# Optimization experiments

Measured on AMD Instinct MI355X. Metric: run time of the kernel, lower is better.

## Reference

```python
import jax, jax.numpy as jnp
import numpy as np

B, S, NX, NH = 4, 1024, 1024, 16
HD = NX // NH  # 64


def setup_inputs() -> dict:
    key = jax.random.key(0)
    k1, k2, k3 = jax.random.split(key, 3)
    return {
        "hidden_states": jax.random.normal(k1, (B, S, NX), dtype=jnp.float32),
        "c_attn_w": jax.random.normal(k2, (NX, 3 * NX), dtype=jnp.float32) * 0.02,
        "c_attn_b": jnp.zeros((3 * NX,), dtype=jnp.float32),
        "c_proj_w": jax.random.normal(k3, (NX, NX), dtype=jnp.float32) * 0.02,
        "c_proj_b": jnp.zeros((NX,), dtype=jnp.float32),
    }


def reference(hidden_states, c_attn_w, c_attn_b, c_proj_w, c_proj_b):
    # Conv1D fused QKV projection: x @ W + b, then split into q,k,v
    qkv = hidden_states @ c_attn_w + c_attn_b  # [B,S,3*NX]
    q, k, v = jnp.split(qkv, 3, axis=-1)
    # split heads -> [B, H, S, D]
    def heads(x):
        return x.reshape(B, S, NH, HD).transpose(0, 2, 1, 3)
    q, k, v = heads(q), heads(k), heads(v)
    # scores: q @ k^T / sqrt(D)  (scale=True; NOTE: no causal mask in this fork)
    w = jnp.einsum("bhqd,bhkd->bhqk", q, k) / jnp.sqrt(jnp.asarray(HD, q.dtype))
    w = jax.nn.softmax(w, axis=-1)
    a = jnp.einsum("bhqk,bhkd->bhqd", w, v)  # [B,H,S,D]
    # merge heads -> [B,S,NX]
    a = a.transpose(0, 2, 1, 3).reshape(B, S, NX)
    # output projection (dropout is identity in eval)
    return a @ c_proj_w + c_proj_b
```

## Files before the change

kernel.cpp:

```cpp
#include <hip/hip_runtime.h>
#include <hip/hip_fp16.h>
#include <cmath>

constexpr int Bb  = 4;
constexpr int Ss  = 1024;
constexpr int NXc = 1024;
constexpr int NHc = 16;
constexpr int HDc = 64;

typedef __bf16    bf16x8 __attribute__((ext_vector_type(8)));
typedef _Float16  f16x8  __attribute__((ext_vector_type(8)));
typedef float     f32x4  __attribute__((ext_vector_type(4)));
typedef unsigned short ushortT;
typedef ushortT ushort8v __attribute__((ext_vector_type(8)));

#define QSCALE 0.18033688011112042f

__device__ __forceinline__ ushortT f2bf_rne(float x) {
  unsigned u = __float_as_uint(x);
  unsigned r = (u + 0x7FFFu + ((u >> 16) & 1u)) >> 16;
  return (ushortT)r;
}
__device__ __forceinline__ ushortT f2h_bits(float x) {
  return __half_as_ushort(__float2half(x));
}
__device__ __forceinline__ float h2f(ushortT h) {
  return __half2float(__ushort_as_half(h));
}
__device__ __forceinline__ void split_f16(float x, ushortT& hi, ushortT& lo) {
  hi = f2h_bits(x);
  lo = f2h_bits(x - h2f(hi));
}

__device__ __forceinline__ void gll16(const void* g, void* l) {
  __builtin_amdgcn_global_load_lds(
      (const __attribute__((address_space(1))) unsigned int*)g,
      (__attribute__((address_space(3))) unsigned int*)l, 16, 0, 0);
}

__device__ __forceinline__ void drain_vmem() {
  asm volatile("s_waitcnt vmcnt(0)" ::: "memory");
  __builtin_amdgcn_sched_barrier(0);
}

__global__ __launch_bounds__(256) void prep_all(
    const float* __restrict__ hs, const float* __restrict__ aw,
    const float* __restrict__ pw,
    ushortT* __restrict__ hF, ushortT* __restrict__ awT,
    ushortT* __restrict__ pwT)
{
  const int bid = blockIdx.x;
  if (bid < 4096) {
    int i = (bid * 256 + threadIdx.x) * 4;
    float4 v = *reinterpret_cast<const float4*>(&hs[i]);
    *reinterpret_cast<ushort4*>(&hF[i]) =
        make_ushort4(f2h_bits(v.x), f2h_bits(v.y), f2h_bits(v.z), f2h_bits(v.w));
    return;
  }
  __shared__ float tile[32][33];
  const int tx = threadIdx.x & 31, ty = threadIdx.x >> 5;
  if (bid < 7168) {
    const int b2 = bid - 4096;
    const int n0 = (b2 % 96) * 32, k0 = (b2 / 96) * 32;
    #pragma unroll
    for (int i = 0; i < 4; ++i)
      tile[ty + i * 8][tx] = aw[(size_t)(k0 + ty + i * 8) * 3072 + n0 + tx];
    __syncthreads();
    #pragma unroll
    for (int i = 0; i < 4; ++i)
      awT[(size_t)(n0 + ty + i * 8) * 1024 + k0 + tx] = f2h_bits(tile[tx][ty + i * 8]);
  } else {
    const int b2 = bid - 7168;
    const int n0 = (b2 & 31) * 32, k0 = (b2 >> 5) * 32;
    #pragma unroll
    for (int i = 0; i < 4; ++i)
      tile[ty + i * 8][tx] = pw[(size_t)(k0 + ty + i * 8) * 1024 + n0 + tx];
    __syncthreads();
    #pragma unroll
    for (int i = 0; i < 4; ++i)
      pwT[(size_t)(n0 + ty + i * 8) * 1024 + k0 + tx] = f2h_bits(tile[tx][ty + i * 8]);
  }
}

__global__ __launch_bounds__(256) void gemm_f16_qkv(
    const ushortT* __restrict__ A16, const ushortT* __restrict__ B16,
    const float* __restrict__ bias,
    ushortT* __restrict__ Qb, ushortT* __restrict__ Kb,
    ushortT* __restrict__ Vt, int M, int N, int K)
{
  constexpr int BK = 64;
  __shared__ ushortT smem[32768];

  const int t    = threadIdx.x;
  const int lane = t & 63;
  const int w    = t >> 6;
  const int wr   = w >> 1, wc = w & 1;
  const int m0 = blockIdx.y * 128;
  const int n0 = blockIdx.x * 128;
  const int l15 = lane & 15;
  const int g   = lane >> 4;

  const int srow  = w * 32 + (lane >> 3);
  const int sslot = (lane & 7) ^ (lane >> 3);

  f32x4 acc[4][4];
  #pragma unroll
  for (int m = 0; m < 4; ++m)
    #pragma unroll
    for (int n = 0; n < 4; ++n)
      #pragma unroll
      for (int r = 0; r < 4; ++r) acc[m][n][r] = 0.f;

  const ushortT* pA = A16 + (size_t)(m0 + srow) * K + sslot * 8;
  const ushortT* pB = B16 + (size_t)(n0 + srow) * K + sslot * 8;

  auto STAGE = [&](ushortT* buf, int k0) {
    #pragma unroll
    for (int i = 0; i < 4; ++i) {
      const size_t gstep = (size_t)i * 8 * K + k0;
      const int    loff  = (w * 32 + i * 8) * BK;
      gll16(pA + gstep, &buf[loff]);
      gll16(pB + gstep, &buf[8192 + loff]);
    }
  };

  const int arow = wr * 64 + l15;
  const int bcol = wc * 64 + l15;

  auto COMPUTE = [&](const ushortT* buf) {
    const ushortT* sA = buf;
    const ushortT* sB = buf + 8192;
    #pragma unroll
    for (int c = 0; c < 2; ++c) {
      const int slot = c * 4 + g;
      f16x8 af[4], bf[4];
      #pragma unroll
      for (int m = 0; m < 4; ++m) {
        int r   = arow + m * 16;
        int off = r * BK + ((slot ^ (r & 7)) * 8);
        af[m] = *reinterpret_cast<const f16x8*>(&sA[off]);
      }
      #pragma unroll
      for (int n = 0; n < 4; ++n) {
        int r   = bcol + n * 16;
        int off = r * BK + ((slot ^ (r & 7)) * 8);
        bf[n] = *reinterpret_cast<const f16x8*>(&sB[off]);
      }
      #pragma unroll
      for (int m = 0; m < 4; ++m)
        #pragma unroll
        for (int n = 0; n < 4; ++n)
          acc[m][n] = __builtin_amdgcn_mfma_f32_16x16x32_f16(af[m], bf[n], acc[m][n], 0, 0, 0);
    }
  };

  const int nt = K / BK;
  STAGE(&smem[0], 0);
  drain_vmem();
  __syncthreads();
  for (int tt = 0; tt < nt; tt += 2) {
    if (tt + 1 < nt) STAGE(&smem[16384], (tt + 1) * BK);
    COMPUTE(&smem[0]);
    drain_vmem();
    __syncthreads();
    if (tt + 2 < nt) STAGE(&smem[0], (tt + 2) * BK);
    COMPUTE(&smem[16384]);
    drain_vmem();
    __syncthreads();
  }

  const int region = n0 >> 10;
  if (region < 2) {
    #pragma unroll
    for (int n = 0; n < 4; ++n) {
      int col_g = n0 + wc * 64 + n * 16 + l15;
      int colm  = col_g & 1023;
      float bv  = bias[col_g];
      #pragma unroll
      for (int m = 0; m < 4; ++m) {
        int row = m0 + wr * 64 + m * 16 + (g << 2);
        #pragma unroll
        for (int r = 0; r < 4; ++r) {
          float v = acc[m][n][r] + bv;
          if (region == 0)
            Qb[(size_t)(row + r) * 1024 + colm] = f2bf_rne(v * QSCALE);
          else
            Kb[(size_t)(row + r) * 1024 + colm] = f2bf_rne(v);
        }
      }
    }
  } else {
    ushortT* T = smem;
    #pragma unroll
    for (int n = 0; n < 4; ++n) {
      int cl   = wc * 64 + n * 16 + l15;
      float bv = bias[n0 + cl];
      #pragma unroll
      for (int m = 0; m < 4; ++m) {
        int rl = wr * 64 + m * 16 + (g << 2);
        #pragma unroll
        for (int r = 0; r < 4; ++r)
          T[cl * 136 + rl + r] = f2bf_rne(acc[m][n][r] + bv);
      }
    }
    __syncthreads();
    const int c  = t >> 1;
    const int rh = (t & 1) * 64;
    const int nn = (n0 - 2048) + c;
    const int hh = nn >> 6, dd = nn & 63;
    const int bb = m0 >> 10;
    const int sl = (m0 & 1023) + rh;
    size_t vbase = ((size_t)((bb * 16 + hh) * 64 + dd)) * 1024 + sl;
    #pragma unroll
    for (int j = 0; j < 8; ++j) {
      ushort8v v = *reinterpret_cast<const ushort8v*>(&T[c * 136 + rh + j * 8]);
      *reinterpret_cast<ushort8v*>(&Vt[vbase + j * 8]) = v;
    }
  }
}

__global__ __launch_bounds__(256) void gemm_f16p2(
    const ushortT* __restrict__ Ah, const ushortT* __restrict__ Al,
    const ushortT* __restrict__ B16,
    const float* __restrict__ bias, float* __restrict__ C,
    int M, int N, int K)
{
  constexpr int BK = 64;
  __shared__ ushortT smem[3 * 8192];
  ushortT* sAh = smem;
  ushortT* sAl = smem + 8192;
  ushortT* sB  = smem + 16384;

  const int t    = threadIdx.x;
  const int lane = t & 63;
  const int w    = t >> 6;
  const int wr   = w >> 1, wc = w & 1;
  const int m0 = blockIdx.y * 128;
  const int n0 = blockIdx.x * 128;
  const int l15 = lane & 15;
  const int g   = lane >> 4;

  const int srow  = w * 32 + (lane >> 3);
  const int sslot = (lane & 7) ^ (lane >> 3);

  f32x4 acc[4][4];
  #pragma unroll
  for (int m = 0; m < 4; ++m)
    #pragma unroll
    for (int n = 0; n < 4; ++n)
      #pragma unroll
      for (int r = 0; r < 4; ++r) acc[m][n][r] = 0.f;

  const ushortT* pAh = Ah  + (size_t)(m0 + srow) * K + sslot * 8;
  const ushortT* pAl = Al  + (size_t)(m0 + srow) * K + sslot * 8;
  const ushortT* pB  = B16 + (size_t)(n0 + srow) * K + sslot * 8;

  for (int k0 = 0; k0 < K; k0 += BK) {
    #pragma unroll
    for (int i = 0; i < 4; ++i) {
      const size_t gstep = (size_t)i * 8 * K + k0;
      const int    loff  = (w * 32 + i * 8) * BK;
      gll16(pAh + gstep, &sAh[loff]);
      gll16(pAl + gstep, &sAl[loff]);
      gll16(pB  + gstep, &sB[loff]);
    }
    __syncthreads();

    const int arow = wr * 64 + l15;
    const int bcol = wc * 64 + l15;
    #pragma unroll
    for (int c = 0; c < 2; ++c) {
      const int slot = c * 4 + g;
      f16x8 afh[4], afl[4], bf[4];
      #pragma unroll
      for (int m = 0; m < 4; ++m) {
        int r   = arow + m * 16;
        int off = r * BK + ((slot ^ (r & 7)) * 8);
        afh[m] = *reinterpret_cast<const f16x8*>(&sAh[off]);
        afl[m] = *reinterpret_cast<const f16x8*>(&sAl[off]);
      }
      #pragma unroll
      for (int n = 0; n < 4; ++n) {
        int r   = bcol + n * 16;
        int off = r * BK + ((slot ^ (r & 7)) * 8);
        bf[n] = *reinterpret_cast<const f16x8*>(&sB[off]);
      }
      #pragma unroll
      for (int m = 0; m < 4; ++m)
        #pragma unroll
        for (int n = 0; n < 4; ++n) {
          acc[m][n] = __builtin_amdgcn_mfma_f32_16x16x32_f16(afh[m], bf[n], acc[m][n], 0, 0, 0);
          acc[m][n] = __builtin_amdgcn_mfma_f32_16x16x32_f16(afl[m], bf[n], acc[m][n], 0, 0, 0);
        }
    }
    __syncthreads();
  }

  #pragma unroll
  for (int n = 0; n < 4; ++n) {
    int col  = n0 + wc * 64 + n * 16 + l15;
    float bv = bias[col];
    #pragma unroll
    for (int m = 0; m < 4; ++m) {
      int row = m0 + wr * 64 + m * 16 + (g << 2);
      #pragma unroll
      for (int r = 0; r < 4; ++r)
        C[(size_t)(row + r) * N + col] = acc[m][n][r] + bv;
    }
  }
}

__global__ __launch_bounds__(256) void attn_mfma(
    const ushortT* __restrict__ Qb, const ushortT* __restrict__ Kb,
    const ushortT* __restrict__ Vt,
    ushortT* __restrict__ aHi, ushortT* __restrict__ aLo)
{
  __shared__ ushortT sK[64 * 64];
  __shared__ ushortT sV[64 * 64];
  __shared__ ushortT sP[64 * 64];

  const int t    = threadIdx.x;
  const int lane = t & 63;
  const int w    = t >> 6;
  const int bh = blockIdx.x, b = bh >> 4, h = bh & 15;
  const int q0 = blockIdx.y * 64;
  const int l15 = lane & 15;
  const int g   = lane >> 4;

  bf16x8 qa[2];
  #pragma unroll
  for (int ks = 0; ks < 2; ++ks) {
    size_t addr = (size_t)(b * 1024 + q0 + w * 16 + l15) * 1024
                  + h * 64 + ks * 32 + g * 8;
    qa[ks] = *reinterpret_cast<const bf16x8*>(&Qb[addr]);
  }

  const int srow  = lane >> 3;
  const int sslot = (lane & 7) ^ srow;

  f32x4 O[4];
  float lp[4];
  #pragma unroll
  for (int r = 0; r < 4; ++r) lp[r] = 0.f;
  #pragma unroll
  for (int n = 0; n < 4; ++n)
    #pragma unroll
    for (int r = 0; r < 4; ++r) O[n][r] = 0.f;

  for (int kt = 0; kt < 16; ++kt) {
    const int k0 = kt * 64;
    #pragma unroll
    for (int i = 0; i < 2; ++i) {
      int r = w * 16 + i * 8 + srow;
      gll16(&Kb[(size_t)(b * 1024 + k0 + r) * 1024 + h * 64 + sslot * 8],
            &sK[(w * 16 + i * 8) * 64]);
      gll16(&Vt[((size_t)bh * 64 + r) * 1024 + k0 + sslot * 8],
            &sV[(w * 16 + i * 8) * 64]);
    }
    __syncthreads();

    f32x4 sc[4];
    #pragma unroll
    for (int n = 0; n < 4; ++n)
      #pragma unroll
      for (int r = 0; r < 4; ++r) sc[n][r] = 0.f;

    #pragma unroll
    for (int ks = 0; ks < 2; ++ks) {
      bf16x8 kb[4];
      #pragma unroll
      for (int n = 0; n < 4; ++n) {
        int row = n * 16 + l15;
        kb[n] = *reinterpret_cast<const bf16x8*>(
            &sK[row * 64 + (((g + ks * 4) ^ (row & 7)) * 8)]);
      }
      #pragma unroll
      for (int n = 0; n < 4; ++n)
        sc[n] = __builtin_amdgcn_mfma_f32_16x16x32_bf16(qa[ks], kb[n], sc[n], 0, 0, 0);
    }

    #pragma unroll
    for (int n = 0; n < 4; ++n)
      #pragma unroll
      for (int r = 0; r < 4; ++r) {
        float p = exp2f(sc[n][r]);
        sc[n][r] = p;
        lp[r] += p;
      }

    #pragma unroll
    for (int n = 0; n < 4; ++n)
      #pragma unroll
      for (int r = 0; r < 4; ++r) {
        int prow = w * 16 + g * 4 + r;
        int c    = n * 16 + l15;
        int off2 = prow * 64 + ((((c >> 3) ^ (prow & 7)) << 3) | (c & 7));
        sP[off2] = f2bf_rne(sc[n][r]);
      }

    #pragma unroll
    for (int ks = 0; ks < 2; ++ks) {
      bf16x8 vb[4], pa;
      #pragma unroll
      for (int n = 0; n < 4; ++n) {
        int rd = n * 16 + l15;
        vb[n] = *reinterpret_cast<const bf16x8*>(
            &sV[rd * 64 + (((g + ks * 4) ^ (rd & 7)) * 8)]);
      }
      {
        int pr = w * 16 + l15;
        pa = *reinterpret_cast<const bf16x8*>(
            &sP[pr * 64 + (((g + ks * 4) ^ (pr & 7)) * 8)]);
      }
      #pragma unroll
      for (int n = 0; n < 4; ++n)
        O[n] = __builtin_amdgcn_mfma_f32_16x16x32_bf16(pa, vb[n], O[n], 0, 0, 0);
    }
    __syncthreads();
  }

  #pragma unroll
  for (int off = 1; off < 16; off <<= 1)
    #pragma unroll
    for (int r = 0; r < 4; ++r)
      lp[r] += __shfl_xor(lp[r], off);

  #pragma unroll
  for (int r = 0; r < 4; ++r) {
    float inv = 1.f / lp[r];
    #pragma unroll
    for (int n = 0; n < 4; ++n) {
      ushortT hi, lo;
      split_f16(O[n][r] * inv, hi, lo);
      size_t off = (size_t)(b * 1024 + q0 + w * 16 + g * 4 + r) * 1024
                   + h * 64 + n * 16 + l15;
      aHi[off] = hi;
      aLo[off] = lo;
    }
  }
}

extern "C" void kernel_launch(void* const* d_in, const int* in_sizes, int n_in,
                              void* d_out, int out_size, void* d_ws, size_t ws_size,
                              hipStream_t stream) {
  const float* hs = (const float*)d_in[0];
  const float* aw = (const float*)d_in[1];
  const float* ab = (const float*)d_in[2];
  const float* pw = (const float*)d_in[3];
  const float* pb = (const float*)d_in[4];
  float* out = (float*)d_out;

  char* ws = (char*)d_ws;
  const int M = Bb * Ss;

  ushortT* hF  = (ushortT*)(ws);
  ushortT* awT = (ushortT*)(ws + ( 8u << 20));
  ushortT* pwT = (ushortT*)(ws + (14u << 20));
  ushortT* Qb  = (ushortT*)(ws + (18u << 20));
  ushortT* Kb  = (ushortT*)(ws + (26u << 20));
  ushortT* Vt  = (ushortT*)(ws + (34u << 20));
  ushortT* xHi = (ushortT*)(ws + (42u << 20));
  ushortT* xLo = (ushortT*)(ws + (50u << 20));

  dim3 blk(256);

  prep_all<<<8192, blk, 0, stream>>>(hs, aw, pw, hF, awT, pwT);
  gemm_f16_qkv<<<dim3(3 * NXc / 128, M / 128), blk, 0, stream>>>(
      hF, awT, ab, Qb, Kb, Vt, M, 3 * NXc, NXc);
  attn_mfma<<<dim3(Bb * NHc, Ss / 64), blk, 0, stream>>>(Qb, Kb, Vt, xHi, xLo);
  gemm_f16p2<<<dim3(NXc / 128, M / 128), blk, 0, stream>>>(
      xHi, xLo, pwT, pb, out, M, NXc, NXc);
}
```

Baseline: 119.5 us.

## Double-buffer K/V tiles in attention and switch intermediates to fp16

Converts the Q, K, V and probability intermediates from bf16 to fp16 and uses fp16 MFMA instructions, improving mantissa precision. The attention kernel now double-buffers K/V tiles in shared memory, issuing the next tile's async global-to-LDS loads before computing the current one, to hide load latency. This doubles K/V LDS usage, which could reduce occupancy. The unnormalized exp values also risk fp16 overflow.

```diff
diff --git a/kernel.cpp b/kernel.cpp
--- a/kernel.cpp
+++ b/kernel.cpp
@@ -16,11 +16,6 @@
 
 #define QSCALE 0.18033688011112042f
 
-__device__ __forceinline__ ushortT f2bf_rne(float x) {
-  unsigned u = __float_as_uint(x);
-  unsigned r = (u + 0x7FFFu + ((u >> 16) & 1u)) >> 16;
-  return (ushortT)r;
-}
 __device__ __forceinline__ ushortT f2h_bits(float x) {
   return __half_as_ushort(__float2half(x));
 }
@@ -183,9 +178,9 @@
         for (int r = 0; r < 4; ++r) {
           float v = acc[m][n][r] + bv;
           if (region == 0)
-            Qb[(size_t)(row + r) * 1024 + colm] = f2bf_rne(v * QSCALE);
+            Qb[(size_t)(row + r) * 1024 + colm] = f2h_bits(v * QSCALE);
           else
-            Kb[(size_t)(row + r) * 1024 + colm] = f2bf_rne(v);
+            Kb[(size_t)(row + r) * 1024 + colm] = f2h_bits(v);
         }
       }
     }
@@ -200,7 +195,7 @@
         int rl = wr * 64 + m * 16 + (g << 2);
         #pragma unroll
         for (int r = 0; r < 4; ++r)
-          T[cl * 136 + rl + r] = f2bf_rne(acc[m][n][r] + bv);
+          T[cl * 136 + rl + r] = f2h_bits(acc[m][n][r] + bv);
       }
     }
     __syncthreads();
@@ -315,8 +310,8 @@
     const ushortT* __restrict__ Vt,
     ushortT* __restrict__ aHi, ushortT* __restrict__ aLo)
 {
-  __shared__ ushortT sK[64 * 64];
-  __shared__ ushortT sV[64 * 64];
+  __shared__ ushortT sK[2][64 * 64];
+  __shared__ ushortT sV[2][64 * 64];
   __shared__ ushortT sP[64 * 64];
 
   const int t    = threadIdx.x;
@@ -327,38 +322,39 @@
   const int l15 = lane & 15;
   const int g   = lane >> 4;
 
-  bf16x8 qa[2];
+  f16x8 qa[2];
   #pragma unroll
   for (int ks = 0; ks < 2; ++ks) {
     size_t addr = (size_t)(b * 1024 + q0 + w * 16 + l15) * 1024
                   + h * 64 + ks * 32 + g * 8;
-    qa[ks] = *reinterpret_cast<const bf16x8*>(&Qb[addr]);
+    qa[ks] = *reinterpret_cast<const f16x8*>(&Qb[addr]);
   }
 
   const int srow  = lane >> 3;
   const int sslot = (lane & 7) ^ srow;
 
-  f32x4 O[4];
-  float lp[4];
-  #pragma unroll
-  for (int r = 0; r < 4; ++r) lp[r] = 0.f;
-  #pragma unroll
-  for (int n = 0; n < 4; ++n)
-    #pragma unroll
-    for (int r = 0; r < 4; ++r) O[n][r] = 0.f;
-
-  for (int kt = 0; kt < 16; ++kt) {
+  auto STAGE = [&](int buf, int kt) {
     const int k0 = kt * 64;
     #pragma unroll
     for (int i = 0; i < 2; ++i) {
       int r = w * 16 + i * 8 + srow;
       gll16(&Kb[(size_t)(b * 1024 + k0 + r) * 1024 + h * 64 + sslot * 8],
-            &sK[(w * 16 + i * 8) * 64]);
+            &sK[buf][(w * 16 + i * 8) * 64]);
       gll16(&Vt[((size_t)bh * 64 + r) * 1024 + k0 + sslot * 8],
-            &sV[(w * 16 + i * 8) * 64]);
-    }
-    __syncthreads();
-
+            &sV[buf][(w * 16 + i * 8) * 64]);
+    }
+  };
+
+  f32x4 O[4];
+  float lp[4];
+  #pragma unroll
+  for (int r = 0; r < 4; ++r) lp[r] = 0.f;
+  #pragma unroll
+  for (int n = 0; n < 4; ++n)
+    #pragma unroll
+    for (int r = 0; r < 4; ++r) O[n][r] = 0.f;
+
+  auto COMPUTE = [&](int buf) {
     f32x4 sc[4];
     #pragma unroll
     for (int n = 0; n < 4; ++n)
@@ -367,16 +363,16 @@
 
     #pragma unroll
     for (int ks = 0; ks < 2; ++ks) {
-      bf16x8 kb[4];
+      f16x8 kb[4];
       #pragma unroll
       for (int n = 0; n < 4; ++n) {
         int row = n * 16 + l15;
-        kb[n] = *reinterpret_cast<const bf16x8*>(
-            &sK[row * 64 + (((g + ks * 4) ^ (row & 7)) * 8)]);
+        kb[n] = *reinterpret_cast<const f16x8*>(
+            &sK[buf][row * 64 + (((g + ks * 4) ^ (row & 7)) * 8)]);
       }
       #pragma unroll
       for (int n = 0; n < 4; ++n)
-        sc[n] = __builtin_amdgcn_mfma_f32_16x16x32_bf16(qa[ks], kb[n], sc[n], 0, 0, 0);
+        sc[n] = __builtin_amdgcn_mfma_f32_16x16x32_f16(qa[ks], kb[n], sc[n], 0, 0, 0);
     }
 
     #pragma unroll
@@ -395,27 +391,40 @@
         int prow = w * 16 + g * 4 + r;
         int c    = n * 16 + l15;
         int off2 = prow * 64 + ((((c >> 3) ^ (prow & 7)) << 3) | (c & 7));
-        sP[off2] = f2bf_rne(sc[n][r]);
+        sP[off2] = f2h_bits(sc[n][r]);
       }
 
     #pragma unroll
     for (int ks = 0; ks < 2; ++ks) {
-      bf16x8 vb[4], pa;
+      f16x8 vb[4], pa;
       #pragma unroll
       for (int n = 0; n < 4; ++n) {
         int rd = n * 16 + l15;
-        vb[n] = *reinterpret_cast<const bf16x8*>(
-            &sV[rd * 64 + (((g + ks * 4) ^ (rd & 7)) * 8)]);
+        vb[n] = *reinterpret_cast<const f16x8*>(
+            &sV[buf][rd * 64 + (((g + ks * 4) ^ (rd & 7)) * 8)]);
       }
       {
         int pr = w * 16 + l15;
-        pa = *reinterpret_cast<const bf16x8*>(
+        pa = *reinterpret_cast<const f16x8*>(
             &sP[pr * 64 + (((g + ks * 4) ^ (pr & 7)) * 8)]);
       }
       #pragma unroll
       for (int n = 0; n < 4; ++n)
-        O[n] = __builtin_amdgcn_mfma_f32_16x16x32_bf16(pa, vb[n], O[n], 0, 0, 0);
-    }
+        O[n] = __builtin_amdgcn_mfma_f32_16x16x32_f16(pa, vb[n], O[n], 0, 0, 0);
+    }
+  };
+
+  STAGE(0, 0);
+  drain_vmem();
+  __syncthreads();
+  for (int kt = 0; kt < 16; kt += 2) {
+    if (kt + 1 < 16) STAGE(1, kt + 1);
+    COMPUTE(0);
+    drain_vmem();
+    __syncthreads();
+    if (kt + 2 < 16) STAGE(0, kt + 2);
+    COMPUTE(1);
+    drain_vmem();
     __syncthreads();
   }
 
```

New measurement: 123.0 us. 1.03x slower.
